# Performance work log

Measured on AMD Instinct MI355X. Metric: run time of the kernel, lower is better.

Reference implementation:

```python
import jax, jax.numpy as jnp
import numpy as np

K = 8
LN_EPS = 1e-5


def setup_inputs() -> dict:
    key = jax.random.key(0)
    ks = jax.random.split(key, 12)
    Nq, N, d = 2048, 50000, 256
    xav = np.sqrt(6.0 / (d + d)).astype(np.float32)
    inp = {
        "query": jax.random.normal(ks[0], (Nq, d), jnp.float32),
        "query_pos": jax.random.uniform(ks[1], (Nq, 3), jnp.float32) * 10.0,
        "inst_feats": jax.random.normal(ks[2], (N, d), jnp.float32),
        "sp_coords": jax.random.uniform(ks[3], (N, 3), jnp.float32) * 10.0,
        "w_q": jax.random.uniform(ks[4], (d, d), jnp.float32, -xav, xav),
        "w_v": jax.random.uniform(ks[5], (d, d), jnp.float32, -xav, xav),
        "w_o": jax.random.uniform(ks[6], (d, d), jnp.float32, -xav, xav),
        # original inits w_k/w_b to zero (uniform gate); use small random for a nontrivial gate
        "w_k": jax.random.normal(ks[7], (K, d), jnp.float32) * 0.02,
        "w_b": jax.random.normal(ks[8], (K,), jnp.float32) * 0.02,
        "gamma": jnp.ones((d,), jnp.float32),
        "beta": jnp.zeros((d,), jnp.float32),
    }
    return inp


def _knn_idx(query_pos, sp_coords, k):
    # squared euclidean distances [Nq, N] via ||q||^2 - 2 q.p + ||p||^2
    d2 = (
        jnp.sum(query_pos * query_pos, -1, keepdims=True)
        - 2.0 * (query_pos @ sp_coords.T)
        + jnp.sum(sp_coords * sp_coords, -1)[None, :]
    )
    _, idx = jax.lax.top_k(-d2, k)  # [Nq, k] nearest-neighbor indices
    return idx


def reference(query, query_pos, inst_feats, sp_coords, w_q, w_v, w_o, w_k, w_b, gamma, beta):
    idx = _knn_idx(query_pos, sp_coords, K)
    feat = inst_feats[idx]                       # [Nq, k, d] gathered neighbor feats
    q = query @ w_q.T                            # [Nq, d]
    v = feat @ w_v.T                             # [Nq, k, d]
    gate = jax.nn.softmax(q @ w_k.T + w_b, -1)   # [Nq, k]
    w = jnp.einsum("qk,qkd->qd", gate, q[:, None, :] * v)
    out = w @ w_o.T + query                      # dropout p=0 -> identity; residual
    mu = jnp.mean(out, -1, keepdims=True)
    var = jnp.mean((out - mu) ** 2, -1, keepdims=True)
    return (out - mu) * jax.lax.rsqrt(var + LN_EPS) * gamma + beta
```

## Files before the change

### kernel.cpp

```cpp
#include <hip/hip_runtime.h>
#include <math.h>

#define D        256
#define KNN      8
#define G        16
#define NCELL    (G*G*G)
#define CS       0.625f
#define EPS_D2   2e-3f
#define CAP      64
#define SPILLMAX 50000

typedef unsigned long long u64;
typedef __attribute__((ext_vector_type(8))) short bf16x8;
typedef __attribute__((ext_vector_type(4))) float f32x4;

__device__ __forceinline__ unsigned short f2b(float f) {
    unsigned u = __float_as_uint(f);
    u += 0x7fff + ((u >> 16) & 1);
    return (unsigned short)(u >> 16);
}
__device__ __forceinline__ bf16x8 pack8(float4 a, float4 b) {
    bf16x8 r;
    r[0] = (short)f2b(a.x); r[1] = (short)f2b(a.y);
    r[2] = (short)f2b(a.z); r[3] = (short)f2b(a.w);
    r[4] = (short)f2b(b.x); r[5] = (short)f2b(b.y);
    r[6] = (short)f2b(b.z); r[7] = (short)f2b(b.w);
    return r;
}

__device__ __forceinline__ unsigned enc_f32(float f) {
    unsigned b = __float_as_uint(f);
    return b ^ ((unsigned)(((int)b) >> 31) | 0x80000000u);
}
__device__ __forceinline__ float dec_f32(unsigned t) {
    unsigned m = (unsigned)(((int)t) >> 31);
    return __uint_as_float(t ^ (0x80000000u | ~m));
}
__device__ __forceinline__ u64 mkkey(float d2, int j) {
    return ((u64)enc_f32(d2) << 32) | (u64)(unsigned)j;
}
__device__ __forceinline__ int cell_of(float x) {
    int c = (int)(x * 1.6f);
    return c < 0 ? 0 : (c > G-1 ? G-1 : c);
}

__global__ __launch_bounds__(256) void prep(const float* __restrict__ w_k,
                                            const float* __restrict__ w_q,
                                            const float* __restrict__ w_v,
                                            const float* __restrict__ w_o,
                                            float* __restrict__ wk2,
                                            unsigned short* __restrict__ wqb,
                                            unsigned short* __restrict__ wvb,
                                            unsigned short* __restrict__ wob,
                                            int4* __restrict__ cnt4,
                                            int* __restrict__ spill_cnt)
{
    const int b = blockIdx.x, t = threadIdx.x;
    if (b < 8) {
        float acc = 0.f;
#pragma unroll 8
        for (int d = 0; d < D; ++d)
            acc = fmaf(w_k[b*D + d], w_q[(size_t)d*D + t], acc);
        wk2[b*D + t] = acc;
    } else if (b < 12) {
        cnt4[(b-8)*256 + t] = make_int4(0, 0, 0, 0);
        if (b == 8 && t == 0) *spill_cnt = 0;
    } else {
        const int m = (b - 12) >> 5;
        const int local = (b - 12) & 31;
        const size_t e = (size_t)local * 2048 + (size_t)t * 8;
        const float* src = (m == 0) ? w_q : (m == 1) ? w_v : w_o;
        unsigned short* dst = (m == 0) ? wqb : (m == 1) ? wvb : wob;
        const float4 x0 = *(const float4*)&src[e];
        const float4 x1 = *(const float4*)&src[e + 4];
        *(bf16x8*)&dst[e] = pack8(x0, x1);
    }
}

__global__ __launch_bounds__(256) void scatter_bins(const float* __restrict__ spc,
                                                    int* __restrict__ cnt,
                                                    float4* __restrict__ bins,
                                                    int* __restrict__ spill_cnt,
                                                    float4* __restrict__ spill, int N)
{
    const int j = blockIdx.x * 256 + threadIdx.x;
    if (j >= N) return;
    const float px = spc[3*j+0], py = spc[3*j+1], pz = spc[3*j+2];
    const int cell = cell_of(px) | (cell_of(py) << 4) | (cell_of(pz) << 8);
    const float4 p = make_float4(px, py, pz, __int_as_float(j));
    const int pos = atomicAdd(&cnt[cell], 1);
    if (pos < CAP) bins[cell*CAP + pos] = p;
    else {
        const int sp = atomicAdd(spill_cnt, 1);
        if (sp < SPILLMAX) spill[sp] = p;
    }
}

#define INSERT8(xk)                                                            \
    if ((xk) < k7) {                                                           \
        const bool c0 = (xk) < k0, c1 = (xk) < k1, c2 = (xk) < k2,             \
                   c3 = (xk) < k3, c4 = (xk) < k4, c5 = (xk) < k5,             \
                   c6 = (xk) < k6;                                             \
        k7 = c6 ? k6 : (xk);                                                   \
        k6 = c5 ? k5 : (c6 ? (xk) : k6);                                       \
        k5 = c4 ? k4 : (c5 ? (xk) : k5);                                       \
        k4 = c3 ? k3 : (c4 ? (xk) : k4);                                       \
        k3 = c2 ? k2 : (c3 ? (xk) : k3);                                       \
        k2 = c1 ? k1 : (c2 ? (xk) : k2);                                       \
        k1 = c0 ? k0 : (c1 ? (xk) : k1);                                       \
        k0 = c0 ? (xk) : k0;                                                   \
    }

#define SCORE(p)                                                               \
    {                                                                          \
        const float sp  = __fadd_rn(__fadd_rn(__fmul_rn((p).x,(p).x),          \
                                  __fmul_rn((p).y,(p).y)), __fmul_rn((p).z,(p).z)); \
        const float dot = __fmaf_rn(qz,(p).z, __fmaf_rn(qy,(p).y, __fmul_rn(qx,(p).x))); \
        const float d2  = __fadd_rn(__fsub_rn(sq, __fmul_rn(2.0f, dot)), sp);  \
        const u64 xk = mkkey(d2, __float_as_int((p).w));                       \
        INSERT8(xk)                                                            \
    }

__device__ __forceinline__ void wave_merge8(int l, u64& k0, u64& k1, u64& k2, u64& k3,
                                            u64& k4, u64& k5, u64& k6, u64& k7,
                                            u64& mine)
{
#pragma unroll
    for (int rd = 0; rd < KNN; ++rd) {
        u64 m = k0;
#pragma unroll
        for (int o = 32; o; o >>= 1) {
            const u64 t = __shfl_xor(m, o);
            if (t < m) m = t;
        }
        if (k0 == m) {
            k0 = k1; k1 = k2; k2 = k3; k3 = k4; k4 = k5; k5 = k6; k6 = k7;
            k7 = ~0ull;
        }
        if (l == rd) mine = m;
    }
}

__global__ __launch_bounds__(512) void mega2(const float* __restrict__ qpos,
                                             const float4* __restrict__ bins,
                                             const int* __restrict__ cnt,
                                             const int* __restrict__ spill_cnt,
                                             const float4* __restrict__ spill,
                                             const float* __restrict__ query,
                                             const float* __restrict__ wk2,
                                             const float* __restrict__ w_b,
                                             const float* __restrict__ feats,
                                             const unsigned short* __restrict__ wqb,
                                             const unsigned short* __restrict__ wvb,
                                             const unsigned short* __restrict__ wob,
                                             const float* __restrict__ gmm,
                                             const float* __restrict__ bta,
                                             float* __restrict__ out)
{
    __shared__ unsigned short a_lds[16][264];
    __shared__ unsigned short f_lds[16][264];
    __shared__ unsigned short w_lds[16][264];
    __shared__ float q_f32[8][260];
    __shared__ float o_f32[8][260];

    const int tid = threadIdx.x;
    const int wv  = tid >> 6, l = tid & 63;
    const int r0  = blockIdx.x * 8;

    {
        const int arr = tid >> 8;
        const int row = 8 + ((tid >> 5) & 7);
        const int o8  = (tid & 31) * 8;
        const bf16x8 z = {0,0,0,0,0,0,0,0};
        if (arr == 0) *(bf16x8*)&a_lds[row][o8] = z;
        else          *(bf16x8*)&f_lds[row][o8] = z;
    }

    {
        const int q = r0 + wv;
        const float qx = qpos[3*q+0], qy = qpos[3*q+1], qz = qpos[3*q+2];
        const float sq = __fadd_rn(__fadd_rn(__fmul_rn(qx,qx), __fmul_rn(qy,qy)),
                                   __fmul_rn(qz,qz));
        const int cx = cell_of(qx), cy = cell_of(qy), cz = cell_of(qz);

        auto bstart = [](int c, float coord) {
            const float f = coord * 1.6f - (float)c;
            int b = c + ((f < 0.5f) ? -2 : -1);
            return b < 0 ? 0 : (b > G-4 ? G-4 : b);
        };
        const int bx = bstart(cx, qx), by = bstart(cy, qy), bz = bstart(cz, qz);

        u64 k0 = ~0ull, k1 = ~0ull, k2 = ~0ull, k3 = ~0ull,
            k4 = ~0ull, k5 = ~0ull, k6 = ~0ull, k7 = ~0ull;

        {
            const int x = bx + (l & 3), y = by + ((l >> 2) & 3), z = bz + (l >> 4);
            const int ci = x | (y << 4) | (z << 8);
            const int n = min(cnt[ci], CAP);
            const int st = ci * CAP;
            for (int i = 0; i < n; ++i) { const float4 p = bins[st + i]; SCORE(p) }
        }
        {
            const int ns = min(*spill_cnt, SPILLMAX);
            for (int i = l; i < ns; i += 64) { const float4 p = spill[i]; SCORE(p) }
        }

        u64 mine = ~0ull;
        wave_merge8(l, k0, k1, k2, k3, k4, k5, k6, k7, mine);
        const u64 worst = __shfl(mine, KNN-1);

        const float w8 = dec_f32((unsigned)(worst >> 32));
        float dmin = INFINITY;
        if (bx > 0)     dmin = fminf(dmin, qx - (float)bx * CS);
        if (bx + 4 < G) dmin = fminf(dmin, (float)(bx + 4) * CS - qx);
        if (by > 0)     dmin = fminf(dmin, qy - (float)by * CS);
        if (by + 4 < G) dmin = fminf(dmin, (float)(by + 4) * CS - qy);
        if (bz > 0)     dmin = fminf(dmin, qz - (float)bz * CS);
        if (bz + 4 < G) dmin = fminf(dmin, (float)(bz + 4) * CS - qz);

        if (!(w8 + EPS_D2 <= dmin * dmin)) {
            k0 = (l < KNN) ? mine : ~0ull;
            k1 = ~0ull; k2 = ~0ull; k3 = ~0ull; k4 = ~0ull;
            k5 = ~0ull; k6 = ~0ull; k7 = ~0ull;
            for (int c = l; c < NCELL; c += 64) {
                const int x = c & 15, y = (c >> 4) & 15, z = c >> 8;
                if (x >= bx && x < bx+4 && y >= by && y < by+4 && z >= bz && z < bz+4) continue;
                const int n = min(cnt[c], CAP);
                const int st = c * CAP;
                for (int i = 0; i < n; ++i) { const float4 p = bins[st + i]; SCORE(p) }
            }
            wave_merge8(l, k0, k1, k2, k3, k4, k5, k6, k7, mine);
        }

        int ids[KNN];
        const int my_id = (int)(unsigned)(mine & 0xffffffffu);
#pragma unroll
        for (int j = 0; j < KNN; ++j) ids[j] = __shfl(my_id, j);

        const float4 qv = *(const float4*)&query[(size_t)q*D + l*4];
        float logit[KNN];
#pragma unroll
        for (int j = 0; j < KNN; ++j) {
            const float4 w = *(const float4*)&wk2[(size_t)j*D + l*4];
            logit[j] = fmaf(qv.x, w.x, fmaf(qv.y, w.y, fmaf(qv.z, w.z, qv.w*w.w)));
        }
#pragma unroll
        for (int o = 32; o; o >>= 1) {
#pragma unroll
            for (int j = 0; j < KNN; ++j) logit[j] += __shfl_xor(logit[j], o);
        }
#pragma unroll
        for (int j = 0; j < KNN; ++j) logit[j] += w_b[j];

        float m = logit[0];
#pragma unroll
        for (int j = 1; j < KNN; ++j) m = fmaxf(m, logit[j]);
        float e[KNN]; float ssum = 0.f;
#pragma unroll
        for (int j = 0; j < KNN; ++j) { e[j] = expf(logit[j] - m); ssum += e[j]; }
        const float inv = 1.f / ssum;

        float4 acc4 = make_float4(0.f, 0.f, 0.f, 0.f);
#pragma unroll
        for (int j = 0; j < KNN; ++j) {
            const float gj = e[j] * inv;
            const float4 f = *(const float4*)&feats[(size_t)ids[j]*D + l*4];
            acc4.x = fmaf(gj, f.x, acc4.x);
            acc4.y = fmaf(gj, f.y, acc4.y);
            acc4.z = fmaf(gj, f.z, acc4.z);
            acc4.w = fmaf(gj, f.w, acc4.w);
        }

        *(float4*)&q_f32[wv][l*4] = qv;
        short4 qb; qb.x = (short)f2b(qv.x); qb.y = (short)f2b(qv.y);
                   qb.z = (short)f2b(qv.z); qb.w = (short)f2b(qv.w);
        *(short4*)&a_lds[wv][l*4] = qb;
        short4 fb; fb.x = (short)f2b(acc4.x); fb.y = (short)f2b(acc4.y);
                   fb.z = (short)f2b(acc4.z); fb.w = (short)f2b(acc4.w);
        *(short4*)&f_lds[wv][l*4] = fb;
    }
    __syncthreads();

    const int mrow = l & 15;
    const int kq   = (l >> 4) * 8;

    f32x4 aq[2], av[2];
#pragma unroll
    for (int t = 0; t < 2; ++t) {
        aq[t] = (f32x4){0.f, 0.f, 0.f, 0.f};
        av[t] = (f32x4){0.f, 0.f, 0.f, 0.f};
    }
#pragma unroll
    for (int k0 = 0; k0 < D; k0 += 32) {
        const bf16x8 af = *(const bf16x8*)&a_lds[mrow][k0 + kq];
        const bf16x8 ff = *(const bf16x8*)&f_lds[mrow][k0 + kq];
#pragma unroll
        for (int t = 0; t < 2; ++t) {
            const int n = wv*32 + t*16 + mrow;
            const bf16x8 bq = *(const bf16x8*)&wqb[(size_t)n*D + k0 + kq];
            const bf16x8 bv = *(const bf16x8*)&wvb[(size_t)n*D + k0 + kq];
            aq[t] = __builtin_amdgcn_mfma_f32_16x16x32_bf16(af, bq, aq[t], 0, 0, 0);
            av[t] = __builtin_amdgcn_mfma_f32_16x16x32_bf16(ff, bv, av[t], 0, 0, 0);
        }
    }

#pragma unroll
    for (int t = 0; t < 2; ++t) {
#pragma unroll
        for (int r = 0; r < 4; ++r) {
            const int row = (l >> 4) * 4 + r;
            const int col = wv*32 + t*16 + (l & 15);
            w_lds[row][col] = f2b(aq[t][r] * av[t][r]);
        }
    }
    __syncthreads();

    f32x4 ao[2];
#pragma unroll
    for (int t = 0; t < 2; ++t) ao[t] = (f32x4){0.f, 0.f, 0.f, 0.f};
#pragma unroll
    for (int k0 = 0; k0 < D; k0 += 32) {
        const bf16x8 wf = *(const bf16x8*)&w_lds[mrow][k0 + kq];
#pragma unroll
        for (int t = 0; t < 2; ++t) {
            const int n = wv*32 + t*16 + mrow;
            const bf16x8 bo = *(const bf16x8*)&wob[(size_t)n*D + k0 + kq];
            ao[t] = __builtin_amdgcn_mfma_f32_16x16x32_bf16(wf, bo, ao[t], 0, 0, 0);
        }
    }
#pragma unroll
    for (int t = 0; t < 2; ++t) {
#pragma unroll
        for (int r = 0; r < 4; ++r) {
            const int row = (l >> 4) * 4 + r;
            if (row < 8) {
                const int col = wv*32 + t*16 + (l & 15);
                o_f32[row][col] = ao[t][r] + q_f32[row][col];
            }
        }
    }
    __syncthreads();

    {
        const float4 v = *(const float4*)&o_f32[wv][l*4];
        float s  = (v.x + v.y) + (v.z + v.w);
        float s2 = fmaf(v.x, v.x, fmaf(v.y, v.y, fmaf(v.z, v.z, v.w*v.w)));
#pragma unroll
        for (int o = 32; o; o >>= 1) { s += __shfl_xor(s, o); s2 += __shfl_xor(s2, o); }
        const float mu  = s * (1.f/256.f);
        const float var = fmaf(s2, 1.f/256.f, -mu*mu);
        const float rs  = rsqrtf(var + 1e-5f);
        const float4 g = *(const float4*)&gmm[l*4];
        const float4 b = *(const float4*)&bta[l*4];
        float4 o4;
        o4.x = (v.x - mu) * rs * g.x + b.x;
        o4.y = (v.y - mu) * rs * g.y + b.y;
        o4.z = (v.z - mu) * rs * g.z + b.z;
        o4.w = (v.w - mu) * rs * g.w + b.w;
        *(float4*)&out[(size_t)(r0+wv)*D + l*4] = o4;
    }
}

extern "C" void kernel_launch(void* const* d_in, const int* in_sizes, int n_in,
                              void* d_out, int out_size, void* d_ws, size_t ws_size,
                              hipStream_t stream)
{
    const float* query = (const float*)d_in[0];
    const float* qpos  = (const float*)d_in[1];
    const float* feats = (const float*)d_in[2];
    const float* spc   = (const float*)d_in[3];
    const float* w_q   = (const float*)d_in[4];
    const float* w_v   = (const float*)d_in[5];
    const float* w_o   = (const float*)d_in[6];
    const float* w_k   = (const float*)d_in[7];
    const float* w_b   = (const float*)d_in[8];
    const float* gamma = (const float*)d_in[9];
    const float* beta  = (const float*)d_in[10];

    const int Nq = in_sizes[0] / D;
    const int N  = in_sizes[2] / D;

    char* ws = (char*)d_ws;
    size_t off = 0;
    int* cnt = (int*)(ws + off);               off += ((size_t)NCELL * 4 + 255) & ~(size_t)255;
    int* spill_cnt = (int*)(ws + off);         off += 256;
    float* wk2 = (float*)(ws + off);           off += ((size_t)KNN * D * 4 + 255) & ~(size_t)255;
    unsigned short* wqb = (unsigned short*)(ws + off); off += (size_t)D * D * 2;
    unsigned short* wvb = (unsigned short*)(ws + off); off += (size_t)D * D * 2;
    unsigned short* wob = (unsigned short*)(ws + off); off += (size_t)D * D * 2;
    float4* bins = (float4*)(ws + off);        off += ((size_t)NCELL * CAP * 16 + 255) & ~(size_t)255;
    float4* spill = (float4*)(ws + off);       off += ((size_t)SPILLMAX * 16 + 255) & ~(size_t)255;

    prep<<<108, 256, 0, stream>>>(w_k, w_q, w_v, w_o, wk2, wqb, wvb, wob,
                                  (int4*)cnt, spill_cnt);
    scatter_bins<<<(N + 255)/256, 256, 0, stream>>>(spc, cnt, bins, spill_cnt, spill, N);
    mega2<<<Nq/8, 512, 0, stream>>>(qpos, bins, cnt, spill_cnt, spill,
                                    query, wk2, w_b, feats, wqb, wvb, wob,
                                    gamma, beta, (float*)d_out);
}
```

Measured before the change: 52.81 us.

## Drop bf16 weight pre-conversion and run 4-query blocks with in-kernel weight packing

Removes the prep-stage conversion of w_q/w_v/w_o to bf16 and instead converts fp32 weights to bf16 fragments on the fly inside the main kernel. Each block now handles 4 queries with 256 threads (4 waves, 64 output columns each) instead of 8 queries with 512 threads, doubling the grid. The KNN+gate logic is factored into a helper function. This saves the prep work, but each block now reads twice the weight bytes in fp32 and does extra conversion ALU. It also doubles total weight traffic because there are more blocks, each covering fewer query rows.

```diff
diff --git a/kernel.cpp b/kernel.cpp
--- a/kernel.cpp
+++ b/kernel.cpp
@@ -42,58 +42,6 @@
 __device__ __forceinline__ int cell_of(float x) {
     int c = (int)(x * 1.6f);
     return c < 0 ? 0 : (c > G-1 ? G-1 : c);
-}
-
-__global__ __launch_bounds__(256) void prep(const float* __restrict__ w_k,
-                                            const float* __restrict__ w_q,
-                                            const float* __restrict__ w_v,
-                                            const float* __restrict__ w_o,
-                                            float* __restrict__ wk2,
-                                            unsigned short* __restrict__ wqb,
-                                            unsigned short* __restrict__ wvb,
-                                            unsigned short* __restrict__ wob,
-                                            int4* __restrict__ cnt4,
-                                            int* __restrict__ spill_cnt)
-{
-    const int b = blockIdx.x, t = threadIdx.x;
-    if (b < 8) {
-        float acc = 0.f;
-#pragma unroll 8
-        for (int d = 0; d < D; ++d)
-            acc = fmaf(w_k[b*D + d], w_q[(size_t)d*D + t], acc);
-        wk2[b*D + t] = acc;
-    } else if (b < 12) {
-        cnt4[(b-8)*256 + t] = make_int4(0, 0, 0, 0);
-        if (b == 8 && t == 0) *spill_cnt = 0;
-    } else {
-        const int m = (b - 12) >> 5;
-        const int local = (b - 12) & 31;
-        const size_t e = (size_t)local * 2048 + (size_t)t * 8;
-        const float* src = (m == 0) ? w_q : (m == 1) ? w_v : w_o;
-        unsigned short* dst = (m == 0) ? wqb : (m == 1) ? wvb : wob;
-        const float4 x0 = *(const float4*)&src[e];
-        const float4 x1 = *(const float4*)&src[e + 4];
-        *(bf16x8*)&dst[e] = pack8(x0, x1);
-    }
-}
-
-__global__ __launch_bounds__(256) void scatter_bins(const float* __restrict__ spc,
-                                                    int* __restrict__ cnt,
-                                                    float4* __restrict__ bins,
-                                                    int* __restrict__ spill_cnt,
-                                                    float4* __restrict__ spill, int N)
-{
-    const int j = blockIdx.x * 256 + threadIdx.x;
-    if (j >= N) return;
-    const float px = spc[3*j+0], py = spc[3*j+1], pz = spc[3*j+2];
-    const int cell = cell_of(px) | (cell_of(py) << 4) | (cell_of(pz) << 8);
-    const float4 p = make_float4(px, py, pz, __int_as_float(j));
-    const int pos = atomicAdd(&cnt[cell], 1);
-    if (pos < CAP) bins[cell*CAP + pos] = p;
-    else {
-        const int sp = atomicAdd(spill_cnt, 1);
-        if (sp < SPILLMAX) spill[sp] = p;
-    }
 }
 
 #define INSERT8(xk)                                                            \
@@ -141,152 +89,216 @@
     }
 }
 
-__global__ __launch_bounds__(512) void mega2(const float* __restrict__ qpos,
-                                             const float4* __restrict__ bins,
-                                             const int* __restrict__ cnt,
-                                             const int* __restrict__ spill_cnt,
-                                             const float4* __restrict__ spill,
-                                             const float* __restrict__ query,
-                                             const float* __restrict__ wk2,
-                                             const float* __restrict__ w_b,
-                                             const float* __restrict__ feats,
-                                             const unsigned short* __restrict__ wqb,
-                                             const unsigned short* __restrict__ wvb,
-                                             const unsigned short* __restrict__ wob,
-                                             const float* __restrict__ gmm,
-                                             const float* __restrict__ bta,
-                                             float* __restrict__ out)
+__global__ __launch_bounds__(256) void prep(const float* __restrict__ w_k,
+                                            const float* __restrict__ w_q,
+                                            float* __restrict__ wk2,
+                                            int4* __restrict__ cnt4,
+                                            int* __restrict__ spill_cnt)
+{
+    const int b = blockIdx.x, t = threadIdx.x;
+    if (b < 8) {
+        float acc = 0.f;
+#pragma unroll 8
+        for (int d = 0; d < D; ++d)
+            acc = fmaf(w_k[b*D + d], w_q[(size_t)d*D + t], acc);
+        wk2[b*D + t] = acc;
+    } else {
+        cnt4[(b-8)*256 + t] = make_int4(0, 0, 0, 0);
+        if (b == 8 && t == 0) *spill_cnt = 0;
+    }
+}
+
+__global__ __launch_bounds__(256) void scatter_bins(const float* __restrict__ spc,
+                                                    int* __restrict__ cnt,
+                                                    float4* __restrict__ bins,
+                                                    int* __restrict__ spill_cnt,
+                                                    float4* __restrict__ spill, int N)
+{
+    const int j = blockIdx.x * 256 + threadIdx.x;
+    if (j >= N) return;
+    const float px = spc[3*j+0], py = spc[3*j+1], pz = spc[3*j+2];
+    const int cell = cell_of(px) | (cell_of(py) << 4) | (cell_of(pz) << 8);
+    const float4 p = make_float4(px, py, pz, __int_as_float(j));
+    const int pos = atomicAdd(&cnt[cell], 1);
+    if (pos < CAP) bins[cell*CAP + pos] = p;
+    else {
+        const int sp = atomicAdd(spill_cnt, 1);
+        if (sp < SPILLMAX) spill[sp] = p;
+    }
+}
+
+__device__ __forceinline__ void knn_gate_wave(int q, int l,
+                                              const float* __restrict__ qpos,
+                                              const float4* __restrict__ bins,
+                                              const int* __restrict__ cnt,
+                                              const int* __restrict__ spill_cnt,
+                                              const float4* __restrict__ spill,
+                                              const float* __restrict__ query,
+                                              const float* __restrict__ wk2,
+                                              const float* __restrict__ w_b,
+                                              const float* __restrict__ feats,
+                                              float4& qv_out, float4& fb_out)
+{
+    const float qx = qpos[3*q+0], qy = qpos[3*q+1], qz = qpos[3*q+2];
+    const float sq = __fadd_rn(__fadd_rn(__fmul_rn(qx,qx), __fmul_rn(qy,qy)),
+                               __fmul_rn(qz,qz));
+    const int cx = cell_of(qx), cy = cell_of(qy), cz = cell_of(qz);
+
+    auto bstart = [](int c, float coord) {
+        const float f = coord * 1.6f - (float)c;
+        int b = c + ((f < 0.5f) ? -2 : -1);
+        return b < 0 ? 0 : (b > G-4 ? G-4 : b);
+    };
+    const int bx = bstart(cx, qx), by = bstart(cy, qy), bz = bstart(cz, qz);
+
+    u64 k0 = ~0ull, k1 = ~0ull, k2 = ~0ull, k3 = ~0ull,
+        k4 = ~0ull, k5 = ~0ull, k6 = ~0ull, k7 = ~0ull;
+
+    {
+        const int x = bx + (l & 3), y = by + ((l >> 2) & 3), z = bz + (l >> 4);
+        const int ci = x | (y << 4) | (z << 8);
+        const int n = min(cnt[ci], CAP);
+        const int st = ci * CAP;
+        for (int i = 0; i < n; ++i) { const float4 p = bins[st + i]; SCORE(p) }
+    }
+    {
+        const int ns = min(*spill_cnt, SPILLMAX);
+        for (int i = l; i < ns; i += 64) { const float4 p = spill[i]; SCORE(p) }
+    }
+
+    u64 mine = ~0ull;
+    wave_merge8(l, k0, k1, k2, k3, k4, k5, k6, k7, mine);
+    const u64 worst = __shfl(mine, KNN-1);
+
+    const float w8 = dec_f32((unsigned)(worst >> 32));
+    float dmin = INFINITY;
+    if (bx > 0)     dmin = fminf(dmin, qx - (float)bx * CS);
+    if (bx + 4 < G) dmin = fminf(dmin, (float)(bx + 4) * CS - qx);
+    if (by > 0)     dmin = fminf(dmin, qy - (float)by * CS);
+    if (by + 4 < G) dmin = fminf(dmin, (float)(by + 4) * CS - qy);
+    if (bz > 0)     dmin = fminf(dmin, qz - (float)bz * CS);
+    if (bz + 4 < G) dmin = fminf(dmin, (float)(bz + 4) * CS - qz);
+
+    if (!(w8 + EPS_D2 <= dmin * dmin)) {
+        k0 = (l < KNN) ? mine : ~0ull;
+        k1 = ~0ull; k2 = ~0ull; k3 = ~0ull; k4 = ~0ull;
+        k5 = ~0ull; k6 = ~0ull; k7 = ~0ull;
+        for (int c = l; c < NCELL; c += 64) {
+            const int x = c & 15, y = (c >> 4) & 15, z = c >> 8;
+            if (x >= bx && x < bx+4 && y >= by && y < by+4 && z >= bz && z < bz+4) continue;
+            const int n = min(cnt[c], CAP);
+            const int st = c * CAP;
+            for (int i = 0; i < n; ++i) { const float4 p = bins[st + i]; SCORE(p) }
+        }
+        wave_merge8(l, k0, k1, k2, k3, k4, k5, k6, k7, mine);
+    }
+
+    int ids[KNN];
+    const int my_id = (int)(unsigned)(mine & 0xffffffffu);
+#pragma unroll
+    for (int j = 0; j < KNN; ++j) ids[j] = __shfl(my_id, j);
+
+    const float4 qv = *(const float4*)&query[(size_t)q*D + l*4];
+    float logit[KNN];
+#pragma unroll
+    for (int j = 0; j < KNN; ++j) {
+        const float4 w = *(const float4*)&wk2[(size_t)j*D + l*4];
+        logit[j] = fmaf(qv.x, w.x, fmaf(qv.y, w.y, fmaf(qv.z, w.z, qv.w*w.w)));
+    }
+#pragma unroll
+    for (int o = 32; o; o >>= 1) {
+#pragma unroll
+        for (int j = 0; j < KNN; ++j) logit[j] += __shfl_xor(logit[j], o);
+    }
+#pragma unroll
+    for (int j = 0; j < KNN; ++j) logit[j] += w_b[j];
+
+    float m = logit[0];
+#pragma unroll
+    for (int j = 1; j < KNN; ++j) m = fmaxf(m, logit[j]);
+    float e[KNN]; float ssum = 0.f;
+#pragma unroll
+    for (int j = 0; j < KNN; ++j) { e[j] = expf(logit[j] - m); ssum += e[j]; }
+    const float inv = 1.f / ssum;
+
+    float4 acc4 = make_float4(0.f, 0.f, 0.f, 0.f);
+#pragma unroll
+    for (int j = 0; j < KNN; ++j) {
+        const float gj = e[j] * inv;
+        const float4 f = *(const float4*)&feats[(size_t)ids[j]*D + l*4];
+        acc4.x = fmaf(gj, f.x, acc4.x);
+        acc4.y = fmaf(gj, f.y, acc4.y);
+        acc4.z = fmaf(gj, f.z, acc4.z);
+        acc4.w = fmaf(gj, f.w, acc4.w);
+    }
+    qv_out = qv;
+    fb_out = acc4;
+}
+
+__device__ __forceinline__ bf16x8 bfrag(const float* __restrict__ w, int n, int k)
+{
+    const float4 a = *(const float4*)&w[(size_t)n*D + k];
+    const float4 b = *(const float4*)&w[(size_t)n*D + k + 4];
+    return pack8(a, b);
+}
+
+__global__ __launch_bounds__(256, 2) void mega3(const float* __restrict__ qpos,
+                                                const float4* __restrict__ bins,
+                                                const int* __restrict__ cnt,
+                                                const int* __restrict__ spill_cnt,
+                                                const float4* __restrict__ spill,
+                                                const float* __restrict__ query,
+                                                const float* __restrict__ wk2,
+                                                const float* __restrict__ w_b,
+                                                const float* __restrict__ feats,
+                                                const float* __restrict__ w_q,
+                                                const float* __restrict__ w_v,
+                                                const float* __restrict__ w_o,
+                                                const float* __restrict__ gmm,
+                                                const float* __restrict__ bta,
+                                                float* __restrict__ out)
 {
     __shared__ unsigned short a_lds[16][264];
     __shared__ unsigned short f_lds[16][264];
     __shared__ unsigned short w_lds[16][264];
-    __shared__ float q_f32[8][260];
-    __shared__ float o_f32[8][260];
+    __shared__ float q_f32[4][260];
+    __shared__ float o_f32[4][260];
 
     const int tid = threadIdx.x;
     const int wv  = tid >> 6, l = tid & 63;
-    const int r0  = blockIdx.x * 8;
+    const int r0  = blockIdx.x * 4;
+
+#pragma unroll
+    for (int k = 0; k < 3; ++k) {
+        const int o = tid + k * 256;
+        const int oo = (o < 384) ? o : o - 384;
+        const int row = 4 + (oo >> 5);
+        const int c8 = (oo & 31) * 8;
+        const bf16x8 z = {0,0,0,0,0,0,0,0};
+        if (o < 384) *(bf16x8*)&a_lds[row][c8] = z;
+        else         *(bf16x8*)&f_lds[row][c8] = z;
+    }
 
     {
-        const int arr = tid >> 8;
-        const int row = 8 + ((tid >> 5) & 7);
-        const int o8  = (tid & 31) * 8;
-        const bf16x8 z = {0,0,0,0,0,0,0,0};
-        if (arr == 0) *(bf16x8*)&a_lds[row][o8] = z;
-        else          *(bf16x8*)&f_lds[row][o8] = z;
-    }
-
-    {
-        const int q = r0 + wv;
-        const float qx = qpos[3*q+0], qy = qpos[3*q+1], qz = qpos[3*q+2];
-        const float sq = __fadd_rn(__fadd_rn(__fmul_rn(qx,qx), __fmul_rn(qy,qy)),
-                                   __fmul_rn(qz,qz));
-        const int cx = cell_of(qx), cy = cell_of(qy), cz = cell_of(qz);
-
-        auto bstart = [](int c, float coord) {
-            const float f = coord * 1.6f - (float)c;
-            int b = c + ((f < 0.5f) ? -2 : -1);
-            return b < 0 ? 0 : (b > G-4 ? G-4 : b);
-        };
-        const int bx = bstart(cx, qx), by = bstart(cy, qy), bz = bstart(cz, qz);
-
-        u64 k0 = ~0ull, k1 = ~0ull, k2 = ~0ull, k3 = ~0ull,
-            k4 = ~0ull, k5 = ~0ull, k6 = ~0ull, k7 = ~0ull;
-
-        {
-            const int x = bx + (l & 3), y = by + ((l >> 2) & 3), z = bz + (l >> 4);
-            const int ci = x | (y << 4) | (z << 8);
-            const int n = min(cnt[ci], CAP);
-            const int st = ci * CAP;
-            for (int i = 0; i < n; ++i) { const float4 p = bins[st + i]; SCORE(p) }
-        }
-        {
-            const int ns = min(*spill_cnt, SPILLMAX);
-            for (int i = l; i < ns; i += 64) { const float4 p = spill[i]; SCORE(p) }
-        }
-
-        u64 mine = ~0ull;
-        wave_merge8(l, k0, k1, k2, k3, k4, k5, k6, k7, mine);
-        const u64 worst = __shfl(mine, KNN-1);
-
-        const float w8 = dec_f32((unsigned)(worst >> 32));
-        float dmin = INFINITY;
-        if (bx > 0)     dmin = fminf(dmin, qx - (float)bx * CS);
-        if (bx + 4 < G) dmin = fminf(dmin, (float)(bx + 4) * CS - qx);
-        if (by > 0)     dmin = fminf(dmin, qy - (float)by * CS);
-        if (by + 4 < G) dmin = fminf(dmin, (float)(by + 4) * CS - qy);
-        if (bz > 0)     dmin = fminf(dmin, qz - (float)bz * CS);
-        if (bz + 4 < G) dmin = fminf(dmin, (float)(bz + 4) * CS - qz);
-
-        if (!(w8 + EPS_D2 <= dmin * dmin)) {
-            k0 = (l < KNN) ? mine : ~0ull;
-            k1 = ~0ull; k2 = ~0ull; k3 = ~0ull; k4 = ~0ull;
-            k5 = ~0ull; k6 = ~0ull; k7 = ~0ull;
-            for (int c = l; c < NCELL; c += 64) {
-                const int x = c & 15, y = (c >> 4) & 15, z = c >> 8;
-                if (x >= bx && x < bx+4 && y >= by && y < by+4 && z >= bz && z < bz+4) continue;
-                const int n = min(cnt[c], CAP);
-                const int st = c * CAP;
-                for (int i = 0; i < n; ++i) { const float4 p = bins[st + i]; SCORE(p) }
-            }
-            wave_merge8(l, k0, k1, k2, k3, k4, k5, k6, k7, mine);
-        }
-
-        int ids[KNN];
-        const int my_id = (int)(unsigned)(mine & 0xffffffffu);
-#pragma unroll
-        for (int j = 0; j < KNN; ++j) ids[j] = __shfl(my_id, j);
-
-        const float4 qv = *(const float4*)&query[(size_t)q*D + l*4];
-        float logit[KNN];
-#pragma unroll
-        for (int j = 0; j < KNN; ++j) {
-            const float4 w = *(const float4*)&wk2[(size_t)j*D + l*4];
-            logit[j] = fmaf(qv.x, w.x, fmaf(qv.y, w.y, fmaf(qv.z, w.z, qv.w*w.w)));
-        }
-#pragma unroll
-        for (int o = 32; o; o >>= 1) {
-#pragma unroll
-            for (int j = 0; j < KNN; ++j) logit[j] += __shfl_xor(logit[j], o);
-        }
-#pragma unroll
-        for (int j = 0; j < KNN; ++j) logit[j] += w_b[j];
-
-        float m = logit[0];
-#pragma unroll
-        for (int j = 1; j < KNN; ++j) m = fmaxf(m, logit[j]);
-        float e[KNN]; float ssum = 0.f;
-#pragma unroll
-        for (int j = 0; j < KNN; ++j) { e[j] = expf(logit[j] - m); ssum += e[j]; }
-        const float inv = 1.f / ssum;
-
-        float4 acc4 = make_float4(0.f, 0.f, 0.f, 0.f);
-#pragma unroll
-        for (int j = 0; j < KNN; ++j) {
-            const float gj = e[j] * inv;
-            const float4 f = *(const float4*)&feats[(size_t)ids[j]*D + l*4];
-            acc4.x = fmaf(gj, f.x, acc4.x);
-            acc4.y = fmaf(gj, f.y, acc4.y);
-            acc4.z = fmaf(gj, f.z, acc4.z);
-            acc4.w = fmaf(gj, f.w, acc4.w);
-        }
-
+        float4 qv, fb;
+        knn_gate_wave(r0 + wv, l, qpos, bins, cnt, spill_cnt, spill,
+                      query, wk2, w_b, feats, qv, fb);
         *(float4*)&q_f32[wv][l*4] = qv;
         short4 qb; qb.x = (short)f2b(qv.x); qb.y = (short)f2b(qv.y);
                    qb.z = (short)f2b(qv.z); qb.w = (short)f2b(qv.w);
         *(short4*)&a_lds[wv][l*4] = qb;
-        short4 fb; fb.x = (short)f2b(acc4.x); fb.y = (short)f2b(acc4.y);
-                   fb.z = (short)f2b(acc4.z); fb.w = (short)f2b(acc4.w);
-        *(short4*)&f_lds[wv][l*4] = fb;
+        short4 fv; fv.x = (short)f2b(fb.x); fv.y = (short)f2b(fb.y);
+                   fv.z = (short)f2b(fb.z); fv.w = (short)f2b(fb.w);
+        *(short4*)&f_lds[wv][l*4] = fv;
     }
     __syncthreads();
 
     const int mrow = l & 15;
     const int kq   = (l >> 4) * 8;
 
-    f32x4 aq[2], av[2];
-#pragma unroll
-    for (int t = 0; t < 2; ++t) {
+    f32x4 aq[4], av[4];
+#pragma unroll
+    for (int t = 0; t < 4; ++t) {
         aq[t] = (f32x4){0.f, 0.f, 0.f, 0.f};
         av[t] = (f32x4){0.f, 0.f, 0.f, 0.f};
     }
@@ -295,46 +307,45 @@
         const bf16x8 af = *(const bf16x8*)&a_lds[mrow][k0 + kq];
         const bf16x8 ff = *(const bf16x8*)&f_lds[mrow][k0 + kq];
 #pragma unroll
-        for (int t = 0; t < 2; ++t) {
-            const int n = wv*32 + t*16 + mrow;
-            const bf16x8 bq = *(const bf16x8*)&wqb[(size_t)n*D + k0 + kq];
-            const bf16x8 bv = *(const bf16x8*)&wvb[(size_t)n*D + k0 + kq];
+        for (int t = 0; t < 4; ++t) {
+            const int n = wv*64 + t*16 + mrow;
+            const bf16x8 bq = bfrag(w_q, n, k0 + kq);
+            const bf16x8 bv = bfrag(w_v, n, k0 + kq);
             aq[t] = __builtin_amdgcn_mfma_f32_16x16x32_bf16(af, bq, aq[t], 0, 0, 0);
             av[t] = __builtin_amdgcn_mfma_f32_16x16x32_bf16(ff, bv, av[t], 0, 0, 0);
         }
     }
-
-#pragma unroll
-    for (int t = 0; t < 2; ++t) {
+#pragma unroll
+    for (int t = 0; t < 4; ++t) {
 #pragma unroll
         for (int r = 0; r < 4; ++r) {
             const int row = (l >> 4) * 4 + r;
-            const int col = wv*32 + t*16 + (l & 15);
+            const int col = wv*64 + t*16 + (l & 15);
             w_lds[row][col] = f2b(aq[t][r] * av[t][r]);
         }
     }
     __syncthreads();
 
-    f32x4 ao[2];
-#pragma unroll
-    for (int t = 0; t < 2; ++t) ao[t] = (f32x4){0.f, 0.f, 0.f, 0.f};
+    f32x4 ao[4];
+#pragma unroll
+    for (int t = 0; t < 4; ++t) ao[t] = (f32x4){0.f, 0.f, 0.f, 0.f};
 #pragma unroll
     for (int k0 = 0; k0 < D; k0 += 32) {
         const bf16x8 wf = *(const bf16x8*)&w_lds[mrow][k0 + kq];
 #pragma unroll
-        for (int t = 0; t < 2; ++t) {
-            const int n = wv*32 + t*16 + mrow;
-            const bf16x8 bo = *(const bf16x8*)&wob[(size_t)n*D + k0 + kq];
+        for (int t = 0; t < 4; ++t) {
+            const int n = wv*64 + t*16 + mrow;
+            const bf16x8 bo = bfrag(w_o, n, k0 + kq);
             ao[t] = __builtin_amdgcn_mfma_f32_16x16x32_bf16(wf, bo, ao[t], 0, 0, 0);
         }
     }
 #pragma unroll
-    for (int t = 0; t < 2; ++t) {
+    for (int t = 0; t < 4; ++t) {
 #pragma unroll
         for (int r = 0; r < 4; ++r) {
             const int row = (l >> 4) * 4 + r;
-            if (row < 8) {
-                const int col = wv*32 + t*16 + (l & 15);
+            if (row < 4) {
+                const int col = wv*64 + t*16 + (l & 15);
                 o_f32[row][col] = ao[t][r] + q_f32[row][col];
             }
         }
@@ -382,19 +393,15 @@
 
     char* ws = (char*)d_ws;
     size_t off = 0;
-    int* cnt = (int*)(ws + off);               off += ((size_t)NCELL * 4 + 255) & ~(size_t)255;
-    int* spill_cnt = (int*)(ws + off);         off += 256;
-    float* wk2 = (float*)(ws + off);           off += ((size_t)KNN * D * 4 + 255) & ~(size_t)255;
-    unsigned short* wqb = (unsigned short*)(ws + off); off += (size_t)D * D * 2;
-    unsigned short* wvb = (unsigned short*)(ws + off); off += (size_t)D * D * 2;
-    unsigned short* wob = (unsigned short*)(ws + off); off += (size_t)D * D * 2;
-    float4* bins = (float4*)(ws + off);        off += ((size_t)NCELL * CAP * 16 + 255) & ~(size_t)255;
-    float4* spill = (float4*)(ws + off);       off += ((size_t)SPILLMAX * 16 + 255) & ~(size_t)255;
-
-    prep<<<108, 256, 0, stream>>>(w_k, w_q, w_v, w_o, wk2, wqb, wvb, wob,
-                                  (int4*)cnt, spill_cnt);
+    int* cnt = (int*)(ws + off);          off += ((size_t)NCELL * 4 + 255) & ~(size_t)255;
+    int* spill_cnt = (int*)(ws + off);    off += 256;
+    float* wk2 = (float*)(ws + off);      off += ((size_t)KNN * D * 4 + 255) & ~(size_t)255;
+    float4* bins = (float4*)(ws + off);   off += ((size_t)NCELL * CAP * 16 + 255) & ~(size_t)255;
+    float4* spill = (float4*)(ws + off);  off += ((size_t)SPILLMAX * 16 + 255) & ~(size_t)255;
+
+    prep<<<12, 256, 0, stream>>>(w_k, w_q, wk2, (int4*)cnt, spill_cnt);
     scatter_bins<<<(N + 255)/256, 256, 0, stream>>>(spc, cnt, bins, spill_cnt, spill, N);
-    mega2<<<Nq/8, 512, 0, stream>>>(qpos, bins, cnt, spill_cnt, spill,
-                                    query, wk2, w_b, feats, wqb, wvb, wob,
+    mega3<<<Nq/4, 256, 0, stream>>>(qpos, bins, cnt, spill_cnt, spill,
+                                    query, wk2, w_b, feats, w_q, w_v, w_o,
                                     gamma, beta, (float*)d_out);
 }
```

Measured after the change: 78.86 us. 49.3% more time.

## Split each query's grid-cell kNN scan across four waves and merge candidates

Applied to the files above, without the earlier changes.

The fused kernel now gives each query four waves instead of one: each wave scans 16 of the 64 neighbourhood cells, with four lanes striding through each cell's points. The four partial top-8 lists are merged through shared memory by one wave. Blocks grow to 1024 threads handling 4 queries, so each wave computes a 16-column slice of the projection GEMMs. The aim is to cut the serial per-lane bin scan latency and raise parallelism, at the cost of padding more of the 16-row MFMA tiles with zeros and adding an extra merge and barrier.

```diff
diff --git a/kernel.cpp b/kernel.cpp
--- a/kernel.cpp
+++ b/kernel.cpp
@@ -42,6 +42,51 @@
 __device__ __forceinline__ int cell_of(float x) {
     int c = (int)(x * 1.6f);
     return c < 0 ? 0 : (c > G-1 ? G-1 : c);
+}
+
+#define INSERT8(xk)                                                            \
+    if ((xk) < k7) {                                                           \
+        const bool c0 = (xk) < k0, c1 = (xk) < k1, c2 = (xk) < k2,             \
+                   c3 = (xk) < k3, c4 = (xk) < k4, c5 = (xk) < k5,             \
+                   c6 = (xk) < k6;                                             \
+        k7 = c6 ? k6 : (xk);                                                   \
+        k6 = c5 ? k5 : (c6 ? (xk) : k6);                                       \
+        k5 = c4 ? k4 : (c5 ? (xk) : k5);                                       \
+        k4 = c3 ? k3 : (c4 ? (xk) : k4);                                       \
+        k3 = c2 ? k2 : (c3 ? (xk) : k3);                                       \
+        k2 = c1 ? k1 : (c2 ? (xk) : k2);                                       \
+        k1 = c0 ? k0 : (c1 ? (xk) : k1);                                       \
+        k0 = c0 ? (xk) : k0;                                                   \
+    }
+
+#define SCORE(p)                                                               \
+    {                                                                          \
+        const float sp  = __fadd_rn(__fadd_rn(__fmul_rn((p).x,(p).x),          \
+                                  __fmul_rn((p).y,(p).y)), __fmul_rn((p).z,(p).z)); \
+        const float dot = __fmaf_rn(qz,(p).z, __fmaf_rn(qy,(p).y, __fmul_rn(qx,(p).x))); \
+        const float d2  = __fadd_rn(__fsub_rn(sq, __fmul_rn(2.0f, dot)), sp);  \
+        const u64 xk = mkkey(d2, __float_as_int((p).w));                       \
+        INSERT8(xk)                                                            \
+    }
+
+__device__ __forceinline__ void wave_merge8(int l, u64& k0, u64& k1, u64& k2, u64& k3,
+                                            u64& k4, u64& k5, u64& k6, u64& k7,
+                                            u64& mine)
+{
+#pragma unroll
+    for (int rd = 0; rd < KNN; ++rd) {
+        u64 m = k0;
+#pragma unroll
+        for (int o = 32; o; o >>= 1) {
+            const u64 t = __shfl_xor(m, o);
+            if (t < m) m = t;
+        }
+        if (k0 == m) {
+            k0 = k1; k1 = k2; k2 = k3; k3 = k4; k4 = k5; k5 = k6; k6 = k7;
+            k7 = ~0ull;
+        }
+        if (l == rd) mine = m;
+    }
 }
 
 __global__ __launch_bounds__(256) void prep(const float* __restrict__ w_k,
@@ -96,119 +141,92 @@
     }
 }
 
-#define INSERT8(xk)                                                            \
-    if ((xk) < k7) {                                                           \
-        const bool c0 = (xk) < k0, c1 = (xk) < k1, c2 = (xk) < k2,             \
-                   c3 = (xk) < k3, c4 = (xk) < k4, c5 = (xk) < k5,             \
-                   c6 = (xk) < k6;                                             \
-        k7 = c6 ? k6 : (xk);                                                   \
-        k6 = c5 ? k5 : (c6 ? (xk) : k6);                                       \
-        k5 = c4 ? k4 : (c5 ? (xk) : k5);                                       \
-        k4 = c3 ? k3 : (c4 ? (xk) : k4);                                       \
-        k3 = c2 ? k2 : (c3 ? (xk) : k3);                                       \
-        k2 = c1 ? k1 : (c2 ? (xk) : k2);                                       \
-        k1 = c0 ? k0 : (c1 ? (xk) : k1);                                       \
-        k0 = c0 ? (xk) : k0;                                                   \
-    }
-
-#define SCORE(p)                                                               \
-    {                                                                          \
-        const float sp  = __fadd_rn(__fadd_rn(__fmul_rn((p).x,(p).x),          \
-                                  __fmul_rn((p).y,(p).y)), __fmul_rn((p).z,(p).z)); \
-        const float dot = __fmaf_rn(qz,(p).z, __fmaf_rn(qy,(p).y, __fmul_rn(qx,(p).x))); \
-        const float d2  = __fadd_rn(__fsub_rn(sq, __fmul_rn(2.0f, dot)), sp);  \
-        const u64 xk = mkkey(d2, __float_as_int((p).w));                       \
-        INSERT8(xk)                                                            \
-    }
-
-__device__ __forceinline__ void wave_merge8(int l, u64& k0, u64& k1, u64& k2, u64& k3,
-                                            u64& k4, u64& k5, u64& k6, u64& k7,
-                                            u64& mine)
-{
-#pragma unroll
-    for (int rd = 0; rd < KNN; ++rd) {
-        u64 m = k0;
-#pragma unroll
-        for (int o = 32; o; o >>= 1) {
-            const u64 t = __shfl_xor(m, o);
-            if (t < m) m = t;
-        }
-        if (k0 == m) {
-            k0 = k1; k1 = k2; k2 = k3; k3 = k4; k4 = k5; k5 = k6; k6 = k7;
-            k7 = ~0ull;
-        }
-        if (l == rd) mine = m;
-    }
-}
-
-__global__ __launch_bounds__(512) void mega2(const float* __restrict__ qpos,
-                                             const float4* __restrict__ bins,
-                                             const int* __restrict__ cnt,
-                                             const int* __restrict__ spill_cnt,
-                                             const float4* __restrict__ spill,
-                                             const float* __restrict__ query,
-                                             const float* __restrict__ wk2,
-                                             const float* __restrict__ w_b,
-                                             const float* __restrict__ feats,
-                                             const unsigned short* __restrict__ wqb,
-                                             const unsigned short* __restrict__ wvb,
-                                             const unsigned short* __restrict__ wob,
-                                             const float* __restrict__ gmm,
-                                             const float* __restrict__ bta,
-                                             float* __restrict__ out)
+__global__ __launch_bounds__(1024, 4) void mega5(const float* __restrict__ qpos,
+                                                 const float4* __restrict__ bins,
+                                                 const int* __restrict__ cnt,
+                                                 const int* __restrict__ spill_cnt,
+                                                 const float4* __restrict__ spill,
+                                                 const float* __restrict__ query,
+                                                 const float* __restrict__ wk2,
+                                                 const float* __restrict__ w_b,
+                                                 const float* __restrict__ feats,
+                                                 const unsigned short* __restrict__ wqb,
+                                                 const unsigned short* __restrict__ wvb,
+                                                 const unsigned short* __restrict__ wob,
+                                                 const float* __restrict__ gmm,
+                                                 const float* __restrict__ bta,
+                                                 float* __restrict__ out)
 {
     __shared__ unsigned short a_lds[16][264];
     __shared__ unsigned short f_lds[16][264];
     __shared__ unsigned short w_lds[16][264];
-    __shared__ float q_f32[8][260];
-    __shared__ float o_f32[8][260];
+    __shared__ float q_f32[4][260];
+    __shared__ float o_f32[4][260];
+    __shared__ u64  cand[4][32];
 
     const int tid = threadIdx.x;
     const int wv  = tid >> 6, l = tid & 63;
-    const int r0  = blockIdx.x * 8;
+    const int qi  = wv >> 2, part = wv & 3;
+    const int r0  = blockIdx.x * 4;
+    const int q   = r0 + qi;
+
+    if (tid < 768) {
+        const int oo = (tid < 384) ? tid : tid - 384;
+        const int row = 4 + (oo >> 5);
+        const int c8 = (oo & 31) * 8;
+        const bf16x8 z = {0,0,0,0,0,0,0,0};
+        if (tid < 384) *(bf16x8*)&a_lds[row][c8] = z;
+        else           *(bf16x8*)&f_lds[row][c8] = z;
+    }
+
+    const float qx = qpos[3*q+0], qy = qpos[3*q+1], qz = qpos[3*q+2];
+    const float sq = __fadd_rn(__fadd_rn(__fmul_rn(qx,qx), __fmul_rn(qy,qy)),
+                               __fmul_rn(qz,qz));
+    const int cx = cell_of(qx), cy = cell_of(qy), cz = cell_of(qz);
+
+    auto bstart = [](int c, float coord) {
+        const float f = coord * 1.6f - (float)c;
+        int b = c + ((f < 0.5f) ? -2 : -1);
+        return b < 0 ? 0 : (b > G-4 ? G-4 : b);
+    };
+    const int bx = bstart(cx, qx), by = bstart(cy, qy), bz = bstart(cz, qz);
+
+    u64 k0 = ~0ull, k1 = ~0ull, k2 = ~0ull, k3 = ~0ull,
+        k4 = ~0ull, k5 = ~0ull, k6 = ~0ull, k7 = ~0ull;
 
     {
-        const int arr = tid >> 8;
-        const int row = 8 + ((tid >> 5) & 7);
-        const int o8  = (tid & 31) * 8;
-        const bf16x8 z = {0,0,0,0,0,0,0,0};
-        if (arr == 0) *(bf16x8*)&a_lds[row][o8] = z;
-        else          *(bf16x8*)&f_lds[row][o8] = z;
-    }
-
-    {
-        const int q = r0 + wv;
-        const float qx = qpos[3*q+0], qy = qpos[3*q+1], qz = qpos[3*q+2];
-        const float sq = __fadd_rn(__fadd_rn(__fmul_rn(qx,qx), __fmul_rn(qy,qy)),
-                                   __fmul_rn(qz,qz));
-        const int cx = cell_of(qx), cy = cell_of(qy), cz = cell_of(qz);
-
-        auto bstart = [](int c, float coord) {
-            const float f = coord * 1.6f - (float)c;
-            int b = c + ((f < 0.5f) ? -2 : -1);
-            return b < 0 ? 0 : (b > G-4 ? G-4 : b);
-        };
-        const int bx = bstart(cx, qx), by = bstart(cy, qy), bz = bstart(cz, qz);
-
-        u64 k0 = ~0ull, k1 = ~0ull, k2 = ~0ull, k3 = ~0ull,
-            k4 = ~0ull, k5 = ~0ull, k6 = ~0ull, k7 = ~0ull;
-
-        {
-            const int x = bx + (l & 3), y = by + ((l >> 2) & 3), z = bz + (l >> 4);
-            const int ci = x | (y << 4) | (z << 8);
-            const int n = min(cnt[ci], CAP);
-            const int st = ci * CAP;
-            for (int i = 0; i < n; ++i) { const float4 p = bins[st + i]; SCORE(p) }
-        }
-        {
-            const int ns = min(*spill_cnt, SPILLMAX);
-            for (int i = l; i < ns; i += 64) { const float4 p = spill[i]; SCORE(p) }
-        }
-
-        u64 mine = ~0ull;
-        wave_merge8(l, k0, k1, k2, k3, k4, k5, k6, k7, mine);
-        const u64 worst = __shfl(mine, KNN-1);
-
+        const int c = part*16 + (l >> 2), sub = l & 3;
+        const int x = bx + (c & 3), y = by + ((c >> 2) & 3), z = bz + (c >> 4);
+        const int ci = x | (y << 4) | (z << 8);
+        const int n = min(cnt[ci], CAP);
+        const int st = ci * CAP;
+        for (int i = sub; i < n; i += 4) { const float4 p = bins[st + i]; SCORE(p) }
+    }
+    if (part == 0) {
+        const int ns = min(*spill_cnt, SPILLMAX);
+        for (int i = l; i < ns; i += 64) { const float4 p = spill[i]; SCORE(p) }
+    }
+
+    u64 mine = ~0ull;
+    wave_merge8(l, k0, k1, k2, k3, k4, k5, k6, k7, mine);
+    if (l < KNN) cand[qi][part*KNN + l] = mine;
+    __syncthreads();
+
+    if (part == 0) {
+        u64 k = (l < 32) ? cand[qi][l] : ~0ull;
+        u64 m2 = ~0ull;
+#pragma unroll
+        for (int rd = 0; rd < KNN; ++rd) {
+            u64 m = k;
+#pragma unroll
+            for (int o = 32; o; o >>= 1) {
+                const u64 t = __shfl_xor(m, o);
+                if (t < m) m = t;
+            }
+            if (k == m) k = ~0ull;
+            if (l == rd) m2 = m;
+        }
+        const u64 worst = __shfl(m2, KNN-1);
         const float w8 = dec_f32((unsigned)(worst >> 32));
         float dmin = INFINITY;
         if (bx > 0)     dmin = fminf(dmin, qx - (float)bx * CS);
@@ -219,7 +237,7 @@
         if (bz + 4 < G) dmin = fminf(dmin, (float)(bz + 4) * CS - qz);
 
         if (!(w8 + EPS_D2 <= dmin * dmin)) {
-            k0 = (l < KNN) ? mine : ~0ull;
+            k0 = (l < KNN) ? m2 : ~0ull;
             k1 = ~0ull; k2 = ~0ull; k3 = ~0ull; k4 = ~0ull;
             k5 = ~0ull; k6 = ~0ull; k7 = ~0ull;
             for (int c = l; c < NCELL; c += 64) {
@@ -229,11 +247,11 @@
                 const int st = c * CAP;
                 for (int i = 0; i < n; ++i) { const float4 p = bins[st + i]; SCORE(p) }
             }
-            wave_merge8(l, k0, k1, k2, k3, k4, k5, k6, k7, mine);
+            wave_merge8(l, k0, k1, k2, k3, k4, k5, k6, k7, m2);
         }
 
         int ids[KNN];
-        const int my_id = (int)(unsigned)(mine & 0xffffffffu);
+        const int my_id = (int)(unsigned)(m2 & 0xffffffffu);
 #pragma unroll
         for (int j = 0; j < KNN; ++j) ids[j] = __shfl(my_id, j);
 
@@ -271,77 +289,57 @@
             acc4.w = fmaf(gj, f.w, acc4.w);
         }
 
-        *(float4*)&q_f32[wv][l*4] = qv;
+        *(float4*)&q_f32[qi][l*4] = qv;
         short4 qb; qb.x = (short)f2b(qv.x); qb.y = (short)f2b(qv.y);
                    qb.z = (short)f2b(qv.z); qb.w = (short)f2b(qv.w);
-        *(short4*)&a_lds[wv][l*4] = qb;
-        short4 fb; fb.x = (short)f2b(acc4.x); fb.y = (short)f2b(acc4.y);
-                   fb.z = (short)f2b(acc4.z); fb.w = (short)f2b(acc4.w);
-        *(short4*)&f_lds[wv][l*4] = fb;
+        *(short4*)&a_lds[qi][l*4] = qb;
+        short4 fv; fv.x = (short)f2b(acc4.x); fv.y = (short)f2b(acc4.y);
+                   fv.z = (short)f2b(acc4.z); fv.w = (short)f2b(acc4.w);
+        *(short4*)&f_lds[qi][l*4] = fv;
     }
     __syncthreads();
 
     const int mrow = l & 15;
     const int kq   = (l >> 4) * 8;
-
-    f32x4 aq[2], av[2];
-#pragma unroll
-    for (int t = 0; t < 2; ++t) {
-        aq[t] = (f32x4){0.f, 0.f, 0.f, 0.f};
-        av[t] = (f32x4){0.f, 0.f, 0.f, 0.f};
-    }
-#pragma unroll
-    for (int k0 = 0; k0 < D; k0 += 32) {
-        const bf16x8 af = *(const bf16x8*)&a_lds[mrow][k0 + kq];
-        const bf16x8 ff = *(const bf16x8*)&f_lds[mrow][k0 + kq];
-#pragma unroll
-        for (int t = 0; t < 2; ++t) {
-            const int n = wv*32 + t*16 + mrow;
-            const bf16x8 bq = *(const bf16x8*)&wqb[(size_t)n*D + k0 + kq];
-            const bf16x8 bv = *(const bf16x8*)&wvb[(size_t)n*D + k0 + kq];
-            aq[t] = __builtin_amdgcn_mfma_f32_16x16x32_bf16(af, bq, aq[t], 0, 0, 0);
-            av[t] = __builtin_amdgcn_mfma_f32_16x16x32_bf16(ff, bv, av[t], 0, 0, 0);
-        }
-    }
-
-#pragma unroll
-    for (int t = 0; t < 2; ++t) {
-#pragma unroll
-        for (int r = 0; r < 4; ++r) {
-            const int row = (l >> 4) * 4 + r;
-            const int col = wv*32 + t*16 + (l & 15);
-            w_lds[row][col] = f2b(aq[t][r] * av[t][r]);
-        }
+    const int ncol = wv*16 + mrow;
+
+    f32x4 aq = (f32x4){0.f, 0.f, 0.f, 0.f};
+    f32x4 av = (f32x4){0.f, 0.f, 0.f, 0.f};
+#pragma unroll
+    for (int k0i = 0; k0i < D; k0i += 32) {
+        const bf16x8 af = *(const bf16x8*)&a_lds[mrow][k0i + kq];
+        const bf16x8 ff = *(const bf16x8*)&f_lds[mrow][k0i + kq];
+        const bf16x8 bq = *(const bf16x8*)&wqb[(size_t)ncol*D + k0i + kq];
+        const bf16x8 bv = *(const bf16x8*)&wvb[(size_t)ncol*D + k0i + kq];
+        aq = __builtin_amdgcn_mfma_f32_16x16x32_bf16(af, bq, aq, 0, 0, 0);
+        av = __builtin_amdgcn_mfma_f32_16x16x32_bf16(ff, bv, av, 0, 0, 0);
+    }
+#pragma unroll
+    for (int r = 0; r < 4; ++r) {
+        const int row = (l >> 4) * 4 + r;
+        const int col = wv*16 + (l & 15);
+        w_lds[row][col] = f2b(aq[r] * av[r]);
     }
     __syncthreads();
 
-    f32x4 ao[2];
-#pragma unroll
-    for (int t = 0; t < 2; ++t) ao[t] = (f32x4){0.f, 0.f, 0.f, 0.f};
-#pragma unroll
-    for (int k0 = 0; k0 < D; k0 += 32) {
-        const bf16x8 wf = *(const bf16x8*)&w_lds[mrow][k0 + kq];
-#pragma unroll
-        for (int t = 0; t < 2; ++t) {
-            const int n = wv*32 + t*16 + mrow;
-            const bf16x8 bo = *(const bf16x8*)&wob[(size_t)n*D + k0 + kq];
-            ao[t] = __builtin_amdgcn_mfma_f32_16x16x32_bf16(wf, bo, ao[t], 0, 0, 0);
-        }
-    }
-#pragma unroll
-    for (int t = 0; t < 2; ++t) {
-#pragma unroll
-        for (int r = 0; r < 4; ++r) {
-            const int row = (l >> 4) * 4 + r;
-            if (row < 8) {
-                const int col = wv*32 + t*16 + (l & 15);
-                o_f32[row][col] = ao[t][r] + q_f32[row][col];
-            }
+    f32x4 ao = (f32x4){0.f, 0.f, 0.f, 0.f};
+#pragma unroll
+    for (int k0i = 0; k0i < D; k0i += 32) {
+        const bf16x8 wf = *(const bf16x8*)&w_lds[mrow][k0i + kq];
+        const bf16x8 bo = *(const bf16x8*)&wob[(size_t)ncol*D + k0i + kq];
+        ao = __builtin_amdgcn_mfma_f32_16x16x32_bf16(wf, bo, ao, 0, 0, 0);
+    }
+#pragma unroll
+    for (int r = 0; r < 4; ++r) {
+        const int row = (l >> 4) * 4 + r;
+        if (row < 4) {
+            const int col = wv*16 + (l & 15);
+            o_f32[row][col] = ao[r] + q_f32[row][col];
         }
     }
     __syncthreads();
 
-    {
+    if (wv < 4) {
         const float4 v = *(const float4*)&o_f32[wv][l*4];
         float s  = (v.x + v.y) + (v.z + v.w);
         float s2 = fmaf(v.x, v.x, fmaf(v.y, v.y, fmaf(v.z, v.z, v.w*v.w)));
@@ -394,7 +392,7 @@
     prep<<<108, 256, 0, stream>>>(w_k, w_q, w_v, w_o, wk2, wqb, wvb, wob,
                                   (int4*)cnt, spill_cnt);
     scatter_bins<<<(N + 255)/256, 256, 0, stream>>>(spc, cnt, bins, spill_cnt, spill, N);
-    mega2<<<Nq/8, 512, 0, stream>>>(qpos, bins, cnt, spill_cnt, spill,
-                                    query, wk2, w_b, feats, wqb, wvb, wob,
-                                    gamma, beta, (float*)d_out);
-}
+    mega5<<<Nq/4, 1024, 0, stream>>>(qpos, bins, cnt, spill_cnt, spill,
+                                     query, wk2, w_b, feats, wqb, wvb, wob,
+                                     gamma, beta, (float*)d_out);
+}
```

After: 71.58 us. 35.5% more time.
